# Kernel tuning notes

Measured on AMD Instinct MI355X. Metric: run time of the kernel, lower is better.

Reference implementation:

```python
import jax, jax.numpy as jnp
import numpy as np

B, S, D, H, DFF = 2, 2048, 768, 12, 3072
DK = D // H
EPS = 1e-6


def setup_inputs() -> dict:
    key = jax.random.key(0)
    ks = jax.random.split(key, 12)
    n = lambda k, shp: jax.random.normal(k, shp, jnp.float32) * 0.02
    return {
        "x": jax.random.normal(ks[0], (B, S, D), jnp.float32),
        "mask": jax.random.randint(ks[1], (1, 1, S, S), 0, 2).astype(jnp.int32),
        "wq": n(ks[2], (D, D)), "bq": jnp.zeros((D,), jnp.float32),
        "wk": n(ks[3], (D, D)), "bk": jnp.zeros((D,), jnp.float32),
        "wv": n(ks[4], (D, D)), "bv": jnp.zeros((D,), jnp.float32),
        "wo": n(ks[5], (D, D)), "bo": jnp.zeros((D,), jnp.float32),
        "w1": n(ks[6], (D, DFF)), "b1": jnp.zeros((DFF,), jnp.float32),
        "w2": n(ks[7], (DFF, D)), "b2": jnp.zeros((D,), jnp.float32),
        "alpha1": jnp.ones((D,), jnp.float32), "beta1": jnp.zeros((D,), jnp.float32),
        "alpha2": jnp.ones((D,), jnp.float32), "beta2": jnp.zeros((D,), jnp.float32),
    }


def _layernorm(x, alpha, bias):
    # Faithful to source: unbiased std (ddof=1) and eps added to std, not var.
    mean = x.mean(axis=-1, keepdims=True)
    var = jnp.sum((x - mean) ** 2, axis=-1, keepdims=True) / (x.shape[-1] - 1)
    return alpha * (x - mean) / (jnp.sqrt(var) + EPS) + bias


def reference(x, mask, wq, bq, wk, bk, wv, bv, wo, bo, w1, b1, w2, b2,
              alpha1, beta1, alpha2, beta2):
    # --- residual 1: pre-norm self-attention ---
    h = _layernorm(x, alpha1, beta1)
    q = (h @ wq + bq).reshape(B, S, H, DK).transpose(0, 2, 1, 3)  # [B,H,S,DK]
    k = (h @ wk + bk).reshape(B, S, H, DK).transpose(0, 2, 1, 3)
    v = (h @ wv + bv).reshape(B, S, H, DK).transpose(0, 2, 1, 3)
    scores = jnp.einsum('bhsd,bhtd->bhst', q, k) / jnp.sqrt(jnp.float32(DK))
    scores = jnp.where(mask == 0, jnp.float32(-1e9), scores)
    attn = jax.nn.softmax(scores, axis=-1)
    o = jnp.einsum('bhst,bhtd->bhsd', attn, v)
    o = o.transpose(0, 2, 1, 3).reshape(B, S, D)
    x = x + (o @ wo + bo)
    # --- residual 2: pre-norm FFN ---
    h2 = _layernorm(x, alpha2, beta2)
    ff = jnp.maximum(h2 @ w1 + b1, 0.0) @ w2 + b2
    return x + ff
```

## Files before the change

### kernel.cpp

```cpp
#include <hip/hip_runtime.h>

typedef unsigned short u16;
typedef unsigned int u32;
typedef unsigned long long u64;
typedef __attribute__((ext_vector_type(8))) short bf16x8;
typedef __attribute__((ext_vector_type(4))) float f32x4;
typedef __attribute__((ext_vector_type(2))) unsigned int u32x2;

#define SEQ 2048
#define DM  768
#define NH  12
#define NB  2
#define LDQ (3 * DM)

#define SCALE_Q 0.180336879f
#define NEGB   -1.44269504e9f

__device__ __forceinline__ float bf2f(u16 u) {
  union { u32 i; float f; } v; v.i = ((u32)u) << 16; return v.f;
}
__device__ __forceinline__ u16 f2bf(float f) {
  union { float f; u32 i; } v; v.f = f;
  u32 r = v.i + 0x7FFFu + ((v.i >> 16) & 1u);
  return (u16)(r >> 16);
}
__device__ __forceinline__ float hw_exp2(float x) {
  float r;
  asm("v_exp_f32 %0, %1" : "=v"(r) : "v"(x));
  return r;
}
__device__ __forceinline__ void gl_lds16(const u16* g, u16* l) {
  __builtin_amdgcn_global_load_lds(
      (const __attribute__((address_space(1))) unsigned int*)g,
      (__attribute__((address_space(3))) unsigned int*)l, 16, 0, 0);
}
template<int N> __device__ __forceinline__ void wait_vmcnt() {
  if constexpr (N == 0) asm volatile("s_waitcnt vmcnt(0)" ::: "memory");
  else if constexpr (N == 3) asm volatile("s_waitcnt vmcnt(3)" ::: "memory");
  else if constexpr (N == 4) asm volatile("s_waitcnt vmcnt(4)" ::: "memory");
  else if constexpr (N == 5) asm volatile("s_waitcnt vmcnt(5)" ::: "memory");
}

__global__ __launch_bounds__(256) void prep_kernel(
    const float* __restrict__ wq, const float* __restrict__ wk,
    const float* __restrict__ wv, const float* __restrict__ wo,
    const float* __restrict__ w1, const float* __restrict__ w2,
    const float* __restrict__ bq, const float* __restrict__ bk,
    const float* __restrict__ bv, const int* __restrict__ mask,
    u16* __restrict__ wqkvt, u16* __restrict__ wot,
    u16* __restrict__ w1t, u16* __restrict__ w2t,
    float* __restrict__ bqkv, u64* __restrict__ mbitsT) {
  __shared__ float t[32][33];
  const int j = blockIdx.x, tid = threadIdx.x;
  const float* in = nullptr; u16* out = nullptr;
  int R = 0, C = 0, bx = 0, by = 0; float sc = 1.0f;
  if (j < 2304) {
    int which = j / 576, local = j % 576;
    in = which == 0 ? wq : which == 1 ? wk : which == 2 ? wv : wo;
    out = which == 3 ? wot : wqkvt + (size_t)which * DM * DM;
    sc = (which == 0) ? SCALE_Q : 1.0f;
    R = DM; C = DM; bx = local % 24; by = local / 24;
  } else if (j < 4608) {
    int local = j - 2304;
    in = w1; out = w1t; R = DM; C = 3072; bx = local % 96; by = local / 96;
  } else if (j < 6912) {
    int local = j - 4608;
    in = w2; out = w2t; R = 3072; C = DM; bx = local % 24; by = local / 24;
  } else if (j < 6921) {
    int i = (j - 6912) * 256 + tid;
    float v = (i < DM) ? bq[i] * SCALE_Q : (i < 2 * DM ? bk[i - DM] : bv[i - 2 * DM]);
    bqkv[i] = v;
    return;
  } else {
    int wid = (j - 6921) * 4 + (tid >> 6);
    int lane = tid & 63;
    int row = wid >> 5, word = wid & 31;
    int m = mask[(long)row * SEQ + word * 64 + lane];
    u64 bb = __ballot(m != 0);
    if (lane == 0) mbitsT[(long)word * SEQ + row] = bb;
    return;
  }
  long r0 = (long)by * 32, c0 = (long)bx * 32;
  int lc = tid & 31, wr = tid >> 5;
#pragma unroll
  for (int i = 0; i < 4; i++) {
    int row = wr + i * 8;
    t[row][lc] = in[(r0 + row) * C + c0 + lc];
  }
  __syncthreads();
#pragma unroll
  for (int i = 0; i < 4; i++) {
    int row = wr + i * 8;
    out[(c0 + row) * R + r0 + lc] = f2bf(t[lc][row] * sc);
  }
}

__global__ __launch_bounds__(256) void transpose_kernel(
    const u16* __restrict__ in, u16* __restrict__ out, int ldin, int R, int C) {
  __shared__ u16 t[32][33];
  long r0 = (long)blockIdx.y * 32, c0 = (long)blockIdx.x * 32;
  int lc = threadIdx.x & 31, wr = threadIdx.x >> 5;
#pragma unroll
  for (int i = 0; i < 4; i++) {
    int row = wr + i * 8;
    t[row][lc] = in[(r0 + row) * (long)ldin + c0 + lc];
  }
  __syncthreads();
#pragma unroll
  for (int i = 0; i < 4; i++) {
    int row = wr + i * 8;
    out[(c0 + row) * R + r0 + lc] = t[lc][row];
  }
}

__global__ __launch_bounds__(256) void ln_kernel(
    const float* __restrict__ x, const float* __restrict__ alpha,
    const float* __restrict__ beta, u16* __restrict__ out) {
  long row = blockIdx.x;
  const float* xr = x + row * DM;
  int tid = threadIdx.x;
  float v[3];
  float s = 0.f, sq = 0.f;
#pragma unroll
  for (int i = 0; i < 3; i++) {
    v[i] = xr[tid + i * 256];
    s += v[i]; sq += v[i] * v[i];
  }
#pragma unroll
  for (int off = 32; off >= 1; off >>= 1) {
    s += __shfl_down(s, off, 64);
    sq += __shfl_down(sq, off, 64);
  }
  __shared__ float ss[4], ssq[4];
  int wave = tid >> 6;
  if ((tid & 63) == 0) { ss[wave] = s; ssq[wave] = sq; }
  __syncthreads();
  float ts = ss[0] + ss[1] + ss[2] + ss[3];
  float tsq = ssq[0] + ssq[1] + ssq[2] + ssq[3];
  float mean = ts * (1.0f / (float)DM);
  float var = fmaxf((tsq - ts * mean) * (1.0f / (float)(DM - 1)), 0.0f);
  float inv = 1.0f / (sqrtf(var) + 1e-6f);
#pragma unroll
  for (int i = 0; i < 3; i++) {
    int c = tid + i * 256;
    out[row * DM + c] = f2bf(alpha[c] * (v[i] - mean) * inv + beta[c]);
  }
}

template<int BN>
__global__ __launch_bounds__(256, 2) void gemm_bt_kernel(
    const u16* __restrict__ A, const u16* __restrict__ Bt,
    const float* __restrict__ bias, const float* res,
    u16* Cb, float* Cf, int M, int N, int K, int relu, int nx) {
  constexpr int NJ = BN / 32;
  constexpr int L = (BN == 128) ? 4 : 3;
  __shared__ __align__(16) u16 As[3][128][32];
  __shared__ __align__(16) u16 Bs[3][BN][32];
  const int tid = threadIdx.x;
  const int lane = tid & 63, wave = tid >> 6;
  const int g = lane >> 4, lr = lane & 15;
  const int wm = (wave >> 1) * 64, wn = (wave & 1) * (BN / 2);
  const int o = blockIdx.x;
  const int wg = (o & 7) * ((int)gridDim.x >> 3) + (o >> 3);
  const int bx = wg % nx, by = wg / nx;
  const long m0 = (long)by * 128;
  const long n0 = (long)bx * BN;
  const int srow = tid >> 2;
  const int scol = (tid & 3) * 8;

  const u16* aSrc = A + (m0 + srow) * K + scol;
  const u16* bSrc = Bt + (n0 + srow) * K + scol;

  auto STAGE = [&](int buf, int t) {
    const int k0 = t * 32;
    gl_lds16(aSrc + k0, &As[buf][srow][scol]);
    gl_lds16(aSrc + (long)64 * K + k0, &As[buf][srow + 64][scol]);
    gl_lds16(bSrc + k0, &Bs[buf][srow][scol]);
    if (BN == 128) gl_lds16(bSrc + (long)64 * K + k0, &Bs[buf][srow + 64][scol]);
  };

  f32x4 acc[4][NJ];
#pragma unroll
  for (int i = 0; i < 4; i++)
#pragma unroll
    for (int j = 0; j < NJ; j++) acc[i][j] = (f32x4)0.0f;

  const int nk = K / 32;
  STAGE(0, 0);
  STAGE(1, 1);
  for (int t = 0; t < nk; t++) {
    const int cur = t % 3;
    if (t + 1 < nk) wait_vmcnt<L>(); else wait_vmcnt<0>();
    __builtin_amdgcn_sched_barrier(0);
    __builtin_amdgcn_s_barrier();
    bf16x8 af[4], bfr[NJ];
#pragma unroll
    for (int i = 0; i < 4; i++) af[i] = *(const bf16x8*)&As[cur][wm + i * 16 + lr][g * 8];
#pragma unroll
    for (int j = 0; j < NJ; j++) bfr[j] = *(const bf16x8*)&Bs[cur][wn + j * 16 + lr][g * 8];
#pragma unroll
    for (int i = 0; i < 4; i++)
#pragma unroll
      for (int j = 0; j < NJ; j++)
        acc[i][j] = __builtin_amdgcn_mfma_f32_16x16x32_bf16(af[i], bfr[j], acc[i][j], 0, 0, 0);
    if (t + 2 < nk) STAGE((t + 2) % 3, t + 2);
  }
#pragma unroll
  for (int j = 0; j < NJ; j++) {
    long col = n0 + wn + j * 16 + lr;
    float bv = bias[col];
#pragma unroll
    for (int i = 0; i < 4; i++) {
#pragma unroll
      for (int r = 0; r < 4; r++) {
        long row = m0 + wm + i * 16 + g * 4 + r;
        float v = acc[i][j][r] + bv;
        if (res) v += res[row * N + col];
        if (relu) v = fmaxf(v, 0.0f);
        if (Cb) Cb[row * N + col] = f2bf(v);
        else    Cf[row * N + col] = v;
      }
    }
  }
}

__global__ __launch_bounds__(256, 3) void attn_kernel(
    const u16* __restrict__ qkv, const u16* __restrict__ vt,
    const u64* __restrict__ mbitsT, u16* __restrict__ o_) {
  __shared__ __align__(16) u16 Ks[2][64][64];
  __shared__ __align__(16) u16 Vs[2][64][64];
  __shared__ __align__(16) u32 Ps32[4][16][36];
  const int o = blockIdx.x;
  const int wg = (o & 7) * 96 + (o >> 3);
  const int qt = wg & 31, h = (wg >> 5) % NH, b = wg / (32 * NH);
  const int tid = threadIdx.x;
  const int lane = tid & 63, wave = tid >> 6;
  const int g = lane >> 4, lr = lane & 15;
  const int qr0 = qt * 64 + wave * 16;
  const int NT = SEQ / 64;

  const u16* q = qkv;
  const u16* k = qkv + DM;

  const long qbase = ((long)(b * SEQ + qr0 + lr)) * LDQ + h * 64;
  bf16x8 qf0 = *(const bf16x8*)(q + qbase + g * 8);
  bf16x8 qf1 = *(const bf16x8*)(q + qbase + 32 + g * 8);

  bf16x8 onesf;
#pragma unroll
  for (int j = 0; j < 8; j++) onesf[j] = (short)0x3F80;

  f32x4 lsum = (f32x4)0.0f;
  f32x4 oacc[4];
#pragma unroll
  for (int d = 0; d < 4; d++) oacc[d] = (f32x4)0.0f;

  const int strow = tid >> 3;
  const int stcolb = (tid & 7) * 16;
  const int swzb = stcolb ^ ((strow & 7) << 4);
  const u16* ksrc = k + (long)b * SEQ * LDQ + h * 64 + (swzb >> 1);
  const u16* vsrc = vt + ((long)(h * 64 + strow)) * (NB * SEQ) + (long)b * SEQ + (swzb >> 1);
  const int sc16 = stcolb >> 1;

  auto STAGE = [&](int buf, int kt) {
    const u16* kr = ksrc + (long)(kt * 64 + strow) * LDQ;
    gl_lds16(kr, &Ks[buf][strow][sc16]);
    gl_lds16(kr + (long)32 * LDQ, &Ks[buf][strow + 32][sc16]);
    const u16* vr = vsrc + kt * 64;
    gl_lds16(vr, &Vs[buf][strow][sc16]);
    gl_lds16(vr + 32 * (NB * SEQ), &Vs[buf][strow + 32][sc16]);
  };

  const int rs = (lr & 7) << 3;
  const int c0 = (g * 8) ^ rs;
  const int c1 = (32 + g * 8) ^ rs;

  const u64* mrow = mbitsT + (qr0 + lr);

  u64 mb_cur = mrow[0];
  STAGE(0, 0);
  for (int kt = 0; kt < NT; kt++) {
    const int cur = kt & 1;
    u64 mb_new = 0;
    if (kt + 1 < NT) {
      mb_new = mrow[(long)(kt + 1) * SEQ];
      STAGE(cur ^ 1, kt + 1);
      wait_vmcnt<5>();
    } else {
      wait_vmcnt<0>();
    }
    __builtin_amdgcn_sched_barrier(0);
    __builtin_amdgcn_s_barrier();

    f32x4 sf[4];
    __builtin_amdgcn_s_setprio(1);
#pragma unroll
    for (int n = 0; n < 4; n++) {
      bf16x8 kb0 = *(const bf16x8*)&Ks[cur][n * 16 + lr][c0];
      bf16x8 kb1 = *(const bf16x8*)&Ks[cur][n * 16 + lr][c1];
      sf[n] = __builtin_amdgcn_mfma_f32_16x16x32_bf16(kb0, qf0, (f32x4)0.0f, 0, 0, 0);
      sf[n] = __builtin_amdgcn_mfma_f32_16x16x32_bf16(kb1, qf1, sf[n], 0, 0, 0);
    }
    __builtin_amdgcn_s_setprio(0);
    u64 tsh = mb_cur >> (4 * g);
    u32 mlo = (u32)tsh, mhi = (u32)(tsh >> 32);
#pragma unroll
    for (int n = 0; n < 4; n++) {
      u32 w = (n < 2) ? mlo : mhi;
#pragma unroll
      for (int r = 0; r < 4; r++) {
        u32 bit = 1u << (16 * (n & 1) + r);
        sf[n][r] = (w & bit) ? sf[n][r] : NEGB;
      }
    }
#pragma unroll
    for (int n = 0; n < 4; n++) {
      union { float f; u32 i; } p0, p1, p2, p3;
      p0.f = hw_exp2(sf[n][0]); p1.f = hw_exp2(sf[n][1]);
      p2.f = hw_exp2(sf[n][2]); p3.f = hw_exp2(sf[n][3]);
      u32 w0 = __builtin_amdgcn_perm(p1.i, p0.i, 0x07060302u);
      u32 w1 = __builtin_amdgcn_perm(p3.i, p2.i, 0x07060302u);
      *(u32x2*)&Ps32[wave][lr][8 * n + 2 * g] = (u32x2){w0, w1};
    }
    asm volatile("" ::: "memory");
    bf16x8 pf0 = *(const bf16x8*)&Ps32[wave][lr][4 * g];
    bf16x8 pf1 = *(const bf16x8*)&Ps32[wave][lr][16 + 4 * g];
    __builtin_amdgcn_s_setprio(1);
    lsum = __builtin_amdgcn_mfma_f32_16x16x32_bf16(onesf, pf0, lsum, 0, 0, 0);
    lsum = __builtin_amdgcn_mfma_f32_16x16x32_bf16(onesf, pf1, lsum, 0, 0, 0);
#pragma unroll
    for (int db = 0; db < 4; db++) {
      bf16x8 v0 = *(const bf16x8*)&Vs[cur][db * 16 + lr][c0];
      bf16x8 v1 = *(const bf16x8*)&Vs[cur][db * 16 + lr][c1];
      oacc[db] = __builtin_amdgcn_mfma_f32_16x16x32_bf16(v0, pf0, oacc[db], 0, 0, 0);
      oacc[db] = __builtin_amdgcn_mfma_f32_16x16x32_bf16(v1, pf1, oacc[db], 0, 0, 0);
    }
    __builtin_amdgcn_s_setprio(0);
    __builtin_amdgcn_sched_barrier(0);
    __builtin_amdgcn_s_barrier();
    mb_cur = mb_new;
  }
  float inv = 1.0f / lsum[0];
  long row = (long)b * SEQ + qr0 + lr;
#pragma unroll
  for (int db = 0; db < 4; db++) {
    u32 lo = ((u32)f2bf(oacc[db][1] * inv) << 16) | f2bf(oacc[db][0] * inv);
    u32 hi = ((u32)f2bf(oacc[db][3] * inv) << 16) | f2bf(oacc[db][2] * inv);
    *(u32x2*)(o_ + row * DM + h * 64 + db * 16 + g * 4) = (u32x2){lo, hi};
  }
}

extern "C" void kernel_launch(void* const* d_in, const int* in_sizes, int n_in,
                              void* d_out, int out_size, void* d_ws, size_t ws_size,
                              hipStream_t stream) {
  const float* x      = (const float*)d_in[0];
  const int*   mask   = (const int*)d_in[1];
  const float* wq     = (const float*)d_in[2];
  const float* bq     = (const float*)d_in[3];
  const float* wk     = (const float*)d_in[4];
  const float* bk     = (const float*)d_in[5];
  const float* wv     = (const float*)d_in[6];
  const float* bv     = (const float*)d_in[7];
  const float* wo     = (const float*)d_in[8];
  const float* bo     = (const float*)d_in[9];
  const float* w1     = (const float*)d_in[10];
  const float* b1     = (const float*)d_in[11];
  const float* w2     = (const float*)d_in[12];
  const float* b2     = (const float*)d_in[13];
  const float* alpha1 = (const float*)d_in[14];
  const float* beta1  = (const float*)d_in[15];
  const float* alpha2 = (const float*)d_in[16];
  const float* beta2  = (const float*)d_in[17];
  float* outf = (float*)d_out;

  char* ws = (char*)d_ws;
  size_t off = 0;
  auto alloc = [&](size_t bytes) {
    void* p = ws + off;
    off += (bytes + 255) & ~(size_t)255;
    return p;
  };
  const size_t DD = (size_t)DM * DM * 2;
  const size_t DF = (size_t)DM * 3072 * 2;
  const size_t ROWS = (size_t)NB * SEQ;
  const size_t ACT = ROWS * DM * 2;

  u16* wqkvt = (u16*)alloc(3 * DD);
  u16* wot   = (u16*)alloc(DD);
  u16* w1t   = (u16*)alloc(DF);
  u16* w2t   = (u16*)alloc(DF);
  float* bqkv = (float*)alloc(3 * DM * 4);
  u64* mbitsT = (u64*)alloc((size_t)(SEQ / 64) * SEQ * 8);
  u16* h     = (u16*)alloc(ACT);
  u16* qkv   = (u16*)alloc(ROWS * 3 * DM * 2);
  u16* vtb   = (u16*)alloc(ACT);
  u16* ob    = (u16*)alloc(ACT);
  u16* fb = qkv;
  u16* h2 = h;
  float* x1 = outf;

  dim3 blk(256);
  prep_kernel<<<dim3(23305), blk, 0, stream>>>(wq, wk, wv, wo, w1, w2, bq, bk, bv,
                                               mask, wqkvt, wot, w1t, w2t, bqkv, mbitsT);

  ln_kernel<<<ROWS, blk, 0, stream>>>(x, alpha1, beta1, h);
  gemm_bt_kernel<128><<<dim3(576), blk, 0, stream>>>(h, wqkvt, bqkv, nullptr, qkv, nullptr, 4096, 3 * DM, 768, 0, 18);
  transpose_kernel<<<dim3(24, 128), blk, 0, stream>>>(qkv + 2 * DM, vtb, LDQ, 4096, 768);
  attn_kernel<<<dim3(32 * NH * NB), blk, 0, stream>>>(qkv, vtb, mbitsT, ob);
  gemm_bt_kernel<64><<<dim3(384), blk, 0, stream>>>(ob, wot, bo, x, nullptr, x1, 4096, 768, 768, 0, 12);
  ln_kernel<<<ROWS, blk, 0, stream>>>(x1, alpha2, beta2, h2);
  gemm_bt_kernel<128><<<dim3(768), blk, 0, stream>>>(h2, w1t, b1, nullptr, fb, nullptr, 4096, 3072, 768, 1, 24);
  gemm_bt_kernel<64><<<dim3(384), blk, 0, stream>>>(fb, w2t, b2, x1, nullptr, outf, 4096, 768, 3072, 0, 12);
}
```

Before: 209.7 us.

## Split-K the FFN down-projection GEMM with atomic accumulation into the output

```diff
diff --git a/kernel.cpp b/kernel.cpp
--- a/kernel.cpp
+++ b/kernel.cpp
@@ -151,7 +151,8 @@
 __global__ __launch_bounds__(256, 2) void gemm_bt_kernel(
     const u16* __restrict__ A, const u16* __restrict__ Bt,
     const float* __restrict__ bias, const float* res,
-    u16* Cb, float* Cf, int M, int N, int K, int relu, int nx) {
+    u16* Cb, float* Cf, int M, int N, int K, int Kld,
+    int relu, int nx, int wgPerChunk) {
   constexpr int NJ = BN / 32;
   constexpr int L = (BN == 128) ? 4 : 3;
   __shared__ __align__(16) u16 As[3][128][32];
@@ -161,22 +162,25 @@
   const int g = lane >> 4, lr = lane & 15;
   const int wm = (wave >> 1) * 64, wn = (wave & 1) * (BN / 2);
   const int o = blockIdx.x;
-  const int wg = (o & 7) * ((int)gridDim.x >> 3) + (o >> 3);
+  int wg = (o & 7) * ((int)gridDim.x >> 3) + (o >> 3);
+  int chunk = 0;
+  if (wgPerChunk) { chunk = wg / wgPerChunk; wg -= chunk * wgPerChunk; }
   const int bx = wg % nx, by = wg / nx;
   const long m0 = (long)by * 128;
   const long n0 = (long)bx * BN;
   const int srow = tid >> 2;
   const int scol = (tid & 3) * 8;
-
-  const u16* aSrc = A + (m0 + srow) * K + scol;
-  const u16* bSrc = Bt + (n0 + srow) * K + scol;
+  const long koff = (long)chunk * K;
+
+  const u16* aSrc = A + (m0 + srow) * Kld + koff + scol;
+  const u16* bSrc = Bt + (n0 + srow) * Kld + koff + scol;
 
   auto STAGE = [&](int buf, int t) {
     const int k0 = t * 32;
     gl_lds16(aSrc + k0, &As[buf][srow][scol]);
-    gl_lds16(aSrc + (long)64 * K + k0, &As[buf][srow + 64][scol]);
+    gl_lds16(aSrc + (long)64 * Kld + k0, &As[buf][srow + 64][scol]);
     gl_lds16(bSrc + k0, &Bs[buf][srow][scol]);
-    if (BN == 128) gl_lds16(bSrc + (long)64 * K + k0, &Bs[buf][srow + 64][scol]);
+    if (BN == 128) gl_lds16(bSrc + (long)64 * Kld + k0, &Bs[buf][srow + 64][scol]);
   };
 
   f32x4 acc[4][NJ];
@@ -208,7 +212,7 @@
 #pragma unroll
   for (int j = 0; j < NJ; j++) {
     long col = n0 + wn + j * 16 + lr;
-    float bv = bias[col];
+    float bv = (bias && chunk == 0) ? bias[col] : 0.0f;
 #pragma unroll
     for (int i = 0; i < 4; i++) {
 #pragma unroll
@@ -217,8 +221,9 @@
         float v = acc[i][j][r] + bv;
         if (res) v += res[row * N + col];
         if (relu) v = fmaxf(v, 0.0f);
-        if (Cb) Cb[row * N + col] = f2bf(v);
-        else    Cf[row * N + col] = v;
+        if (wgPerChunk) atomicAdd(&Cf[row * N + col], v);
+        else if (Cb)    Cb[row * N + col] = f2bf(v);
+        else            Cf[row * N + col] = v;
       }
     }
   }
@@ -404,11 +409,15 @@
                                                mask, wqkvt, wot, w1t, w2t, bqkv, mbitsT);
 
   ln_kernel<<<ROWS, blk, 0, stream>>>(x, alpha1, beta1, h);
-  gemm_bt_kernel<128><<<dim3(576), blk, 0, stream>>>(h, wqkvt, bqkv, nullptr, qkv, nullptr, 4096, 3 * DM, 768, 0, 18);
+  gemm_bt_kernel<128><<<dim3(576), blk, 0, stream>>>(
+      h, wqkvt, bqkv, nullptr, qkv, nullptr, 4096, 3 * DM, 768, 768, 0, 18, 0);
   transpose_kernel<<<dim3(24, 128), blk, 0, stream>>>(qkv + 2 * DM, vtb, LDQ, 4096, 768);
   attn_kernel<<<dim3(32 * NH * NB), blk, 0, stream>>>(qkv, vtb, mbitsT, ob);
-  gemm_bt_kernel<64><<<dim3(384), blk, 0, stream>>>(ob, wot, bo, x, nullptr, x1, 4096, 768, 768, 0, 12);
+  gemm_bt_kernel<64><<<dim3(384), blk, 0, stream>>>(
+      ob, wot, bo, x, nullptr, x1, 4096, 768, 768, 768, 0, 12, 0);
   ln_kernel<<<ROWS, blk, 0, stream>>>(x1, alpha2, beta2, h2);
-  gemm_bt_kernel<128><<<dim3(768), blk, 0, stream>>>(h2, w1t, b1, nullptr, fb, nullptr, 4096, 3072, 768, 1, 24);
-  gemm_bt_kernel<64><<<dim3(384), blk, 0, stream>>>(fb, w2t, b2, x1, nullptr, outf, 4096, 768, 3072, 0, 12);
-}
+  gemm_bt_kernel<128><<<dim3(768), blk, 0, stream>>>(
+      h2, w1t, b1, nullptr, fb, nullptr, 4096, 3072, 768, 768, 1, 24, 0);
+  gemm_bt_kernel<64><<<dim3(768), blk, 0, stream>>>(
+      fb, w2t, b2, nullptr, nullptr, outf, 4096, 768, 1536, 3072, 0, 12, 384);
+}
```

Measured after the change: 208.0 us. No clear change (-0.8%).
